# Kernel optimization log

Measured on AMD Instinct MI355X. Metric: run time of the kernel, lower is better.

## Reference

```python
import jax, jax.numpy as jnp
import numpy as np

EMB_DIM = 768
HEADS = 12
HEAD_DIM = EMB_DIM // HEADS  # 64


def setup_inputs() -> dict:
    key = jax.random.key(0)
    ks = jax.random.split(key, 9)
    s = 1.0 / np.sqrt(EMB_DIM)
    d = dict(
        x=jax.random.normal(ks[0], (2, 2048, EMB_DIM), dtype=jnp.float32),
        wq_w=jax.random.normal(ks[1], (EMB_DIM, EMB_DIM), dtype=jnp.float32) * s,
        wq_b=jax.random.normal(ks[2], (EMB_DIM,), dtype=jnp.float32) * 0.01,
        wk_w=jax.random.normal(ks[3], (EMB_DIM, EMB_DIM), dtype=jnp.float32) * s,
        wk_b=jax.random.normal(ks[4], (EMB_DIM,), dtype=jnp.float32) * 0.01,
        wv_w=jax.random.normal(ks[5], (EMB_DIM, EMB_DIM), dtype=jnp.float32) * s,
        wv_b=jax.random.normal(ks[6], (EMB_DIM,), dtype=jnp.float32) * 0.01,
        wo_w=jax.random.normal(ks[7], (EMB_DIM, EMB_DIM), dtype=jnp.float32) * s,
        wo_b=jax.random.normal(ks[8], (EMB_DIM,), dtype=jnp.float32) * 0.01,
    )
    return d


def reference(x, wq_w, wq_b, wk_w, wk_b, wv_w, wv_b, wo_w, wo_b):
    b, n, _ = x.shape
    # Linear projections (torch Linear: x @ W^T + b). q scaled by 1/8 == 1/sqrt(head_dim).
    q = (x @ wq_w.T + wq_b) / 8.0
    k = x @ wk_w.T + wk_b
    v = x @ wv_w.T + wv_b
    # [b, h, n, d]
    q = q.reshape(b, n, HEADS, HEAD_DIM).transpose(0, 2, 1, 3)
    k = k.reshape(b, n, HEADS, HEAD_DIM).transpose(0, 2, 1, 3)
    v = v.reshape(b, n, HEADS, HEAD_DIM).transpose(0, 2, 1, 3)
    # Full [b, h, n, n] score matrix with causal mask (strict upper triangle = -inf)
    scores = jnp.einsum('bhqd,bhkd->bhqk', q, k)
    causal = jnp.tril(jnp.ones((n, n), dtype=bool))  # True where allowed
    scores = jnp.where(causal[None, None], scores, -jnp.inf)
    attn = jax.nn.softmax(scores, axis=-1)
    out = jnp.einsum('bhqk,bhkd->bhqd', attn, v)
    out = out.transpose(0, 2, 1, 3).reshape(b, n, EMB_DIM)
    return out @ wo_w.T + wo_b
```

## Files before the change

### kernel.cpp

```cpp
#include <hip/hip_runtime.h>
#include <hip/hip_bf16.h>
#include <math.h>

#define EMB  768
#define NH   12
#define HD   64
#define SEQ  2048
#define BATCH 2
#define NTOK 4096

typedef __attribute__((ext_vector_type(8))) short short8;
typedef __attribute__((ext_vector_type(4))) float float4v;

static __device__ __forceinline__ short f2bf(float f) {
    __hip_bfloat16 h = __float2bfloat16(f);
    return *reinterpret_cast<short*>(&h);
}

static __device__ __forceinline__ void gll16(const void* g, void* l) {
    __builtin_amdgcn_global_load_lds(
        (const __attribute__((address_space(1))) void*)g,
        (__attribute__((address_space(3))) void*)l, 16, 0, 0);
}

__device__ const unsigned char UB[40] = {
    3,4,5,6,7,8,9,10,11,12,13,14,15,
    7,8,9,10,11,12,13,14,15,
    11,12,13,14,15,
    15,
    2,6,10,14,
    1,5,9,13,
    0,4,8,12};
__device__ const unsigned char UC[40] = {
    0,0,0,0,0,0,0,0,0,0,0,0,0,
    1,1,1,1,1,1,1,1,1,
    2,2,2,2,2,
    3,
    0,1,2,3,
    0,1,2,3,
    0,1,2,3};

__global__ __launch_bounds__(256) void cast_kernel(
    const float* __restrict__ x,  const float* __restrict__ wq,
    const float* __restrict__ wk, const float* __restrict__ wv,
    const float* __restrict__ wo,
    __hip_bfloat16* __restrict__ xb,  __hip_bfloat16* __restrict__ wqb,
    __hip_bfloat16* __restrict__ wkb, __hip_bfloat16* __restrict__ wvb,
    __hip_bfloat16* __restrict__ wob)
{
    const size_t S0 = (size_t)NTOK * EMB;
    const size_t S1 = (size_t)EMB * EMB;
    size_t i = ((size_t)blockIdx.x * 256 + threadIdx.x) * 8;
    const float* src; __hip_bfloat16* dst; size_t off;
    if      (i < S0)            { src = x;  dst = xb;  off = i; }
    else if (i < S0 + S1)       { src = wq; dst = wqb; off = i - S0; }
    else if (i < S0 + 2 * S1)   { src = wk; dst = wkb; off = i - S0 - S1; }
    else if (i < S0 + 3 * S1)   { src = wv; dst = wvb; off = i - S0 - 2 * S1; }
    else                        { src = wo; dst = wob; off = i - S0 - 3 * S1; }
    float4 f0 = *(const float4*)&src[off];
    float4 f1 = *(const float4*)&src[off + 4];
    short8 o;
    o[0] = f2bf(f0.x); o[1] = f2bf(f0.y); o[2] = f2bf(f0.z); o[3] = f2bf(f0.w);
    o[4] = f2bf(f1.x); o[5] = f2bf(f1.y); o[6] = f2bf(f1.z); o[7] = f2bf(f1.w);
    *(short8*)&dst[off] = o;
}

__global__ __launch_bounds__(256) void qkv_mfma_kernel(
    const __hip_bfloat16* __restrict__ xb,
    const __hip_bfloat16* __restrict__ wqb, const float* __restrict__ bq,
    const __hip_bfloat16* __restrict__ wkb, const float* __restrict__ bk,
    const __hip_bfloat16* __restrict__ wvb, const float* __restrict__ bv,
    __hip_bfloat16* __restrict__ q, __hip_bfloat16* __restrict__ k,
    __hip_bfloat16* __restrict__ vT)
{
    __shared__ __align__(16) short SM[12288];
    short* As = SM;
    short* Bs = SM + 4096;
    const int t = threadIdx.x;
    const int w = t >> 6, lane = t & 63;
    const int col = lane & 15, quad = lane >> 4;
    const int wm = w >> 1, wn = w & 1;
    const int m0 = blockIdx.y * 64;
    const int mat = blockIdx.x / 6;
    const int jj0 = (blockIdx.x % 6) * 128;
    const short* X = (const short*)xb;
    const short* W = (const short*)((mat == 0) ? wqb : (mat == 1) ? wkb : wvb);
    const float* bias = (mat == 0) ? bq : (mat == 1) ? bk : bv;

    float4v acc[2][4];
    #pragma unroll
    for (int mi = 0; mi < 2; ++mi)
        #pragma unroll
        for (int ni = 0; ni < 4; ++ni) acc[mi][ni] = (float4v){0.f, 0.f, 0.f, 0.f};

    for (int kb = 0; kb < EMB; kb += 64) {
        #pragma unroll
        for (int c = 0; c < 2; ++c) {
            int I = w * 128 + c * 64 + lane;
            int row = I >> 3;
            int c8 = (I & 7) ^ (row & 7);
            gll16(X + (size_t)(m0 + row) * EMB + kb + c8 * 8,
                  &As[(w * 128 + c * 64) * 8]);
        }
        #pragma unroll
        for (int c = 0; c < 4; ++c) {
            int I = w * 256 + c * 64 + lane;
            int row = I >> 3;
            int c8 = (I & 7) ^ (row & 7);
            gll16(W + (size_t)(jj0 + row) * EMB + kb + c8 * 8,
                  &Bs[(w * 256 + c * 64) * 8]);
        }
        __syncthreads();
        #pragma unroll
        for (int ks = 0; ks < 2; ++ks) {
            short8 a[2], b[4];
            #pragma unroll
            for (int mi = 0; mi < 2; ++mi) {
                int row = wm * 32 + mi * 16 + col;
                a[mi] = *(short8*)&As[row * 64 + (((ks * 4 + quad) ^ (row & 7)) * 8)];
            }
            #pragma unroll
            for (int ni = 0; ni < 4; ++ni) {
                int row = wn * 64 + ni * 16 + col;
                b[ni] = *(short8*)&Bs[row * 64 + (((ks * 4 + quad) ^ (row & 7)) * 8)];
            }
            #pragma unroll
            for (int mi = 0; mi < 2; ++mi)
                #pragma unroll
                for (int ni = 0; ni < 4; ++ni)
                    acc[mi][ni] = __builtin_amdgcn_mfma_f32_16x16x32_bf16(
                        a[mi], b[ni], acc[mi][ni], 0, 0, 0);
        }
        __syncthreads();
    }
    const int bi = m0 >> 11, n0g = m0 & (SEQ - 1);
    if (mat != 2) {
        const float scale = (mat == 0) ? 0.125f * 1.44269504088896f : 1.0f;
        __hip_bfloat16* dstqk = (mat == 0) ? q : k;
        #pragma unroll
        for (int mi = 0; mi < 2; ++mi)
            #pragma unroll
            for (int ni = 0; ni < 4; ++ni) {
                int gj_l = wn * 64 + ni * 16 + col;
                float bsv = bias[jj0 + gj_l];
                #pragma unroll
                for (int r = 0; r < 4; ++r) {
                    int n_l = wm * 32 + mi * 16 + quad * 4 + r;
                    int cswz = (gj_l >> 3) ^ (n_l & 15);
                    SM[(n_l << 7) + (cswz << 3) + (gj_l & 7)] =
                        f2bf((acc[mi][ni][r] + bsv) * scale);
                }
            }
        __syncthreads();
        #pragma unroll
        for (int it = 0; it < 4; ++it) {
            int I = it * 256 + t;
            int n_l = I >> 4, c = I & 15;
            short8 val = *(short8*)&SM[(n_l << 7) + ((c ^ (n_l & 15)) << 3)];
            int gj = jj0 + c * 8;
            int h = gj >> 6, d0 = gj & 63;
            int gm = m0 + n_l;
            int bb = gm >> 11, n = gm & (SEQ - 1);
            *(short8*)&dstqk[(((size_t)bb * NH + h) * SEQ + n) * HD + d0] = val;
        }
    } else {
        #pragma unroll
        for (int mi = 0; mi < 2; ++mi)
            #pragma unroll
            for (int ni = 0; ni < 4; ++ni) {
                int d_l = wn * 64 + ni * 16 + col;
                float bsv = bias[jj0 + d_l];
                #pragma unroll
                for (int r = 0; r < 4; ++r) {
                    int n_l = wm * 32 + mi * 16 + quad * 4 + r;
                    int cn = n_l >> 3;
                    SM[(d_l << 6) + (((cn ^ (d_l & 7))) << 3) + (n_l & 7)] =
                        f2bf(acc[mi][ni][r] + bsv);
                }
            }
        __syncthreads();
        #pragma unroll
        for (int it = 0; it < 4; ++it) {
            int I = it * 256 + t;
            int d_l = I >> 3, cn = I & 7;
            short8 val = *(short8*)&SM[(d_l << 6) + ((cn ^ (d_l & 7)) << 3)];
            int gj = jj0 + d_l;
            int h = gj >> 6, dd = gj & 63;
            *(short8*)&vT[(((size_t)bi * NH + h) * HD + dd) * SEQ + n0g + cn * 8] = val;
        }
    }
}

__global__ __launch_bounds__(256) void attn_mfma_kernel(
    const __hip_bfloat16* __restrict__ qg, const __hip_bfloat16* __restrict__ kg,
    const __hip_bfloat16* __restrict__ vTg, __hip_bfloat16* __restrict__ ao,
    float* __restrict__ Osp, float* __restrict__ lsp)
{
    __shared__ __align__(16) short Ks[2][64 * 64];
    __shared__ __align__(16) short Vt[2][64 * 64];
    __shared__ __align__(16) short Ps[4][32][72];
    const int t = threadIdx.x;
    const int w = t >> 6, lane = t & 63;
    const int col = lane & 15, quad = lane >> 4;
    const int id = blockIdx.x;
    const int bh = id % 24;
    const int x = id / 24;
    const int b = UB[x], c = UC[x];
    const int kt0 = c * 8;
    const int tottiles = 2 * b + 2;
    const int niter = (tottiles - kt0 < 8) ? (tottiles - kt0) : 8;
    const bool single = (b <= 3);
    const int q0 = b * 128;
    const size_t base = (size_t)bh * SEQ * HD;
    const short* kp = (const short*)kg + base;
    const short* vp = (const short*)vTg + base;
    const short* qp = (const short*)qg + base;

    short8 qa[2][2];
    #pragma unroll
    for (int mi = 0; mi < 2; ++mi) {
        int qrow = q0 + (2 * w + mi) * 16 + col;
        #pragma unroll
        for (int ks = 0; ks < 2; ++ks)
            qa[mi][ks] = *(const short8*)&qp[(size_t)qrow * HD + ks * 32 + quad * 8];
    }
    float4v accO[2][4];
    float lacc[2][4];
    #pragma unroll
    for (int mi = 0; mi < 2; ++mi) {
        #pragma unroll
        for (int di = 0; di < 4; ++di) accO[mi][di] = (float4v){0.f, 0.f, 0.f, 0.f};
        #pragma unroll
        for (int r = 0; r < 4; ++r) lacc[mi][r] = 0.f;
    }

    {
        const int k0 = kt0 * 64;
        #pragma unroll
        for (int cc = 0; cc < 2; ++cc) {
            int I = w * 128 + cc * 64 + lane;
            int row = I >> 3;
            int c8 = (I & 7) ^ (row & 7);
            gll16(kp + (size_t)(k0 + row) * HD + c8 * 8, &Ks[0][(w * 128 + cc * 64) * 8]);
            gll16(vp + (size_t)row * SEQ + k0 + c8 * 8, &Vt[0][(w * 128 + cc * 64) * 8]);
        }
    }

    for (int lk = 0; lk < niter; ++lk) {
        const int kt = kt0 + lk;
        const int cur = lk & 1;
        const int k0 = kt * 64;
        __syncthreads();
        if (lk + 1 < niter) {
            const int kn = k0 + 64;
            #pragma unroll
            for (int cc = 0; cc < 2; ++cc) {
                int I = w * 128 + cc * 64 + lane;
                int row = I >> 3;
                int c8 = (I & 7) ^ (row & 7);
                gll16(kp + (size_t)(kn + row) * HD + c8 * 8,
                      &Ks[cur ^ 1][(w * 128 + cc * 64) * 8]);
                gll16(vp + (size_t)row * SEQ + kn + c8 * 8,
                      &Vt[cur ^ 1][(w * 128 + cc * 64) * 8]);
            }
        }
        const short* Kc = &Ks[cur][0];
        const short* Vc = &Vt[cur][0];

        float4v s[2][4];
        #pragma unroll
        for (int mi = 0; mi < 2; ++mi)
            #pragma unroll
            for (int ni = 0; ni < 4; ++ni) s[mi][ni] = (float4v){0.f, 0.f, 0.f, 0.f};
        #pragma unroll
        for (int ks = 0; ks < 2; ++ks)
            #pragma unroll
            for (int ni = 0; ni < 4; ++ni) {
                int row = ni * 16 + col;
                short8 kf = *(short8*)&Kc[row * 64 + (((ks * 4 + quad) ^ (row & 7)) * 8)];
                #pragma unroll
                for (int mi = 0; mi < 2; ++mi)
                    s[mi][ni] = __builtin_amdgcn_mfma_f32_16x16x32_bf16(
                        qa[mi][ks], kf, s[mi][ni], 0, 0, 0);
            }

        if (k0 >= q0) {
            #pragma unroll
            for (int mi = 0; mi < 2; ++mi)
                #pragma unroll
                for (int ni = 0; ni < 4; ++ni) {
                    int gcol = k0 + ni * 16 + col;
                    #pragma unroll
                    for (int r = 0; r < 4; ++r) {
                        int grow = q0 + (2 * w + mi) * 16 + quad * 4 + r;
                        s[mi][ni][r] = (gcol > grow) ? 0.f : exp2f(s[mi][ni][r]);
                    }
                }
        } else {
            #pragma unroll
            for (int mi = 0; mi < 2; ++mi)
                #pragma unroll
                for (int ni = 0; ni < 4; ++ni)
                    #pragma unroll
                    for (int r = 0; r < 4; ++r)
                        s[mi][ni][r] = exp2f(s[mi][ni][r]);
        }
        #pragma unroll
        for (int mi = 0; mi < 2; ++mi)
            #pragma unroll
            for (int r = 0; r < 4; ++r)
                lacc[mi][r] += (s[mi][0][r] + s[mi][1][r]) + (s[mi][2][r] + s[mi][3][r]);

        #pragma unroll
        for (int mi = 0; mi < 2; ++mi)
            #pragma unroll
            for (int ni = 0; ni < 4; ++ni)
                #pragma unroll
                for (int r = 0; r < 4; ++r)
                    Ps[w][mi * 16 + quad * 4 + r][ni * 16 + col] = f2bf(s[mi][ni][r]);
        short8 pa[2][2];
        #pragma unroll
        for (int mi = 0; mi < 2; ++mi)
            #pragma unroll
            for (int ks = 0; ks < 2; ++ks)
                pa[mi][ks] = *(short8*)&Ps[w][mi * 16 + col][ks * 32 + quad * 8];

        #pragma unroll
        for (int ks = 0; ks < 2; ++ks)
            #pragma unroll
            for (int di = 0; di < 4; ++di) {
                int row = di * 16 + col;
                short8 vf = *(short8*)&Vc[row * 64 + (((ks * 4 + quad) ^ (row & 7)) * 8)];
                #pragma unroll
                for (int mi = 0; mi < 2; ++mi)
                    accO[mi][di] = __builtin_amdgcn_mfma_f32_16x16x32_bf16(
                        pa[mi][ks], vf, accO[mi][di], 0, 0, 0);
            }
    }

    #pragma unroll
    for (int msk = 1; msk < 16; msk <<= 1)
        #pragma unroll
        for (int mi = 0; mi < 2; ++mi)
            #pragma unroll
            for (int r = 0; r < 4; ++r)
                lacc[mi][r] += __shfl_xor(lacc[mi][r], msk);

    const int bi = bh / NH, h = bh % NH;
    if (single) {
        #pragma unroll
        for (int mi = 0; mi < 2; ++mi)
            #pragma unroll
            for (int r = 0; r < 4; ++r) {
                float inv = 1.0f / lacc[mi][r];
                int n = q0 + (2 * w + mi) * 16 + quad * 4 + r;
                #pragma unroll
                for (int di = 0; di < 4; ++di)
                    ao[((size_t)bi * SEQ + n) * EMB + h * HD + di * 16 + col] =
                        __float2bfloat16(accO[mi][di][r] * inv);
            }
    } else {
        float* Os = Osp + (size_t)c * 2 * 1536 * EMB;
        float* ls = lsp + (size_t)c * 2 * 1536 * NH;
        #pragma unroll
        for (int mi = 0; mi < 2; ++mi)
            #pragma unroll
            for (int r = 0; r < 4; ++r) {
                int n = q0 + (2 * w + mi) * 16 + quad * 4 + r;
                int nn = n - 512;
                size_t rowb = ((size_t)bi * 1536 + nn) * EMB + h * HD;
                #pragma unroll
                for (int di = 0; di < 4; ++di)
                    Os[rowb + di * 16 + col] = accO[mi][di][r];
                if (col == 0)
                    ls[((size_t)bi * 1536 + nn) * NH + h] = lacc[mi][r];
            }
    }
}

__global__ __launch_bounds__(256) void combine_kernel(
    const float* __restrict__ Osp, const float* __restrict__ lsp,
    __hip_bfloat16* __restrict__ ao)
{
    const size_t SLOT = (size_t)2 * 1536 * EMB;
    const size_t LSLOT = (size_t)2 * 1536 * NH;
    size_t e8 = ((size_t)blockIdx.x * 256 + threadIdx.x) * 8;
    int u = e8 / EMB;
    int within = e8 % EMB;
    int h = within >> 6;
    int bi = u / 1536, nn = u % 1536;
    int n = 512 + nn;
    int qb = n >> 7;
    int nc = (2 * qb + 9) >> 3;
    float4 a0 = *(const float4*)&Osp[e8];
    float4 a1 = *(const float4*)&Osp[e8 + 4];
    float lsum = lsp[(size_t)u * NH + h];
    for (int cc = 1; cc < nc; ++cc) {
        const float* O = Osp + (size_t)cc * SLOT;
        float4 b0 = *(const float4*)&O[e8];
        float4 b1 = *(const float4*)&O[e8 + 4];
        a0.x += b0.x; a0.y += b0.y; a0.z += b0.z; a0.w += b0.w;
        a1.x += b1.x; a1.y += b1.y; a1.z += b1.z; a1.w += b1.w;
        lsum += lsp[(size_t)cc * LSLOT + (size_t)u * NH + h];
    }
    float inv = 1.0f / lsum;
    short8 o;
    o[0] = f2bf(a0.x * inv); o[1] = f2bf(a0.y * inv);
    o[2] = f2bf(a0.z * inv); o[3] = f2bf(a0.w * inv);
    o[4] = f2bf(a1.x * inv); o[5] = f2bf(a1.y * inv);
    o[6] = f2bf(a1.z * inv); o[7] = f2bf(a1.w * inv);
    *(short8*)&ao[((size_t)bi * SEQ + n) * EMB + within] = o;
}

__global__ __launch_bounds__(256) void out_proj_mfma_kernel(
    const __hip_bfloat16* __restrict__ a, const __hip_bfloat16* __restrict__ wob,
    const float* __restrict__ bias, float* __restrict__ out)
{
    __shared__ __align__(16) short As[64 * 64];
    __shared__ __align__(16) short Bs[64 * 64];
    const int t = threadIdx.x;
    const int w = t >> 6, lane = t & 63;
    const int col = lane & 15, quad = lane >> 4;
    const int wm = w >> 1, wn = w & 1;
    const int m0 = blockIdx.y * 64;
    const int n0 = blockIdx.x * 64;
    const short* A = (const short*)a;
    const short* W = (const short*)wob;

    float4v acc[2][2];
    #pragma unroll
    for (int mi = 0; mi < 2; ++mi)
        #pragma unroll
        for (int ni = 0; ni < 2; ++ni) acc[mi][ni] = (float4v){0.f, 0.f, 0.f, 0.f};

    for (int kb = 0; kb < EMB; kb += 64) {
        #pragma unroll
        for (int c = 0; c < 2; ++c) {
            int I = w * 128 + c * 64 + lane;
            int row = I >> 3;
            int c8 = (I & 7) ^ (row & 7);
            gll16(A + (size_t)(m0 + row) * EMB + kb + c8 * 8,
                  &As[(w * 128 + c * 64) * 8]);
            gll16(W + (size_t)(n0 + row) * EMB + kb + c8 * 8,
                  &Bs[(w * 128 + c * 64) * 8]);
        }
        __syncthreads();
        #pragma unroll
        for (int ks = 0; ks < 2; ++ks) {
            short8 av[2], bv[2];
            #pragma unroll
            for (int mi = 0; mi < 2; ++mi) {
                int row = wm * 32 + mi * 16 + col;
                av[mi] = *(short8*)&As[row * 64 + (((ks * 4 + quad) ^ (row & 7)) * 8)];
            }
            #pragma unroll
            for (int ni = 0; ni < 2; ++ni) {
                int row = wn * 32 + ni * 16 + col;
                bv[ni] = *(short8*)&Bs[row * 64 + (((ks * 4 + quad) ^ (row & 7)) * 8)];
            }
            #pragma unroll
            for (int mi = 0; mi < 2; ++mi)
                #pragma unroll
                for (int ni = 0; ni < 2; ++ni)
                    acc[mi][ni] = __builtin_amdgcn_mfma_f32_16x16x32_bf16(
                        av[mi], bv[ni], acc[mi][ni], 0, 0, 0);
        }
        __syncthreads();
    }
    #pragma unroll
    for (int mi = 0; mi < 2; ++mi)
        #pragma unroll
        for (int ni = 0; ni < 2; ++ni) {
            int gj = n0 + wn * 32 + ni * 16 + col;
            float bsv = bias[gj];
            #pragma unroll
            for (int r = 0; r < 4; ++r) {
                int gm = m0 + wm * 32 + mi * 16 + quad * 4 + r;
                out[(size_t)gm * EMB + gj] = acc[mi][ni][r] + bsv;
            }
        }
}

extern "C" void kernel_launch(void* const* d_in, const int* in_sizes, int n_in,
                              void* d_out, int out_size, void* d_ws, size_t ws_size,
                              hipStream_t stream) {
    const float* x  = (const float*)d_in[0];
    const float* wq = (const float*)d_in[1];
    const float* bq = (const float*)d_in[2];
    const float* wk = (const float*)d_in[3];
    const float* bk = (const float*)d_in[4];
    const float* wv = (const float*)d_in[5];
    const float* bv = (const float*)d_in[6];
    const float* wo = (const float*)d_in[7];
    const float* bo = (const float*)d_in[8];
    float* out = (float*)d_out;

    const size_t TOK = (size_t)NTOK * EMB;
    const size_t WSZ = (size_t)EMB * EMB;
    __hip_bfloat16* xb  = (__hip_bfloat16*)d_ws;
    __hip_bfloat16* wqb = xb  + TOK;
    __hip_bfloat16* wkb = wqb + WSZ;
    __hip_bfloat16* wvb = wkb + WSZ;
    __hip_bfloat16* wob = wvb + WSZ;
    __hip_bfloat16* qb  = wob + WSZ;
    __hip_bfloat16* kb  = qb  + TOK;
    __hip_bfloat16* vTb = kb  + TOK;
    __hip_bfloat16* aob = vTb + TOK;
    float* Osp = (float*)(aob + TOK);
    float* lsp = Osp + (size_t)4 * 2 * 1536 * EMB;

    cast_kernel<<<2688, 256, 0, stream>>>(x, wq, wk, wv, wo, xb, wqb, wkb, wvb, wob);
    qkv_mfma_kernel<<<dim3(18, 64), 256, 0, stream>>>(xb, wqb, bq, wkb, bk, wvb, bv,
                                                      qb, kb, vTb);
    attn_mfma_kernel<<<960, 256, 0, stream>>>(qb, kb, vTb, aob, Osp, lsp);
    combine_kernel<<<1152, 256, 0, stream>>>(Osp, lsp, aob);
    out_proj_mfma_kernel<<<dim3(12, 64), 256, 0, stream>>>(aob, wob, bo, out);
}
```

Baseline: 160.6 us.

## Fuse split-KV combine into output projection A-tile loading

Removes the separate combine kernel. For rows that have split partial results, the output projection kernel now sums the fp32 partial O slots and l sums itself, normalizes, converts to bf16 and writes the A tile into LDS. This saves one launch and the bf16 round trip through global memory. In exchange, every column block re-reads and re-reduces the fp32 partials, so partial-buffer traffic grows about twelvefold, and these A loads become synchronous register loads instead of direct-to-LDS loads.

Measured after the change: 192.3 us. +19.7%, slower.

```diff
diff --git a/kernel.cpp b/kernel.cpp
--- a/kernel.cpp
+++ b/kernel.cpp
@@ -378,54 +378,43 @@
     }
 }
 
-__global__ __launch_bounds__(256) void combine_kernel(
-    const float* __restrict__ Osp, const float* __restrict__ lsp,
-    __hip_bfloat16* __restrict__ ao)
-{
-    const size_t SLOT = (size_t)2 * 1536 * EMB;
-    const size_t LSLOT = (size_t)2 * 1536 * NH;
-    size_t e8 = ((size_t)blockIdx.x * 256 + threadIdx.x) * 8;
-    int u = e8 / EMB;
-    int within = e8 % EMB;
-    int h = within >> 6;
-    int bi = u / 1536, nn = u % 1536;
-    int n = 512 + nn;
-    int qb = n >> 7;
-    int nc = (2 * qb + 9) >> 3;
-    float4 a0 = *(const float4*)&Osp[e8];
-    float4 a1 = *(const float4*)&Osp[e8 + 4];
-    float lsum = lsp[(size_t)u * NH + h];
-    for (int cc = 1; cc < nc; ++cc) {
-        const float* O = Osp + (size_t)cc * SLOT;
-        float4 b0 = *(const float4*)&O[e8];
-        float4 b1 = *(const float4*)&O[e8 + 4];
-        a0.x += b0.x; a0.y += b0.y; a0.z += b0.z; a0.w += b0.w;
-        a1.x += b1.x; a1.y += b1.y; a1.z += b1.z; a1.w += b1.w;
-        lsum += lsp[(size_t)cc * LSLOT + (size_t)u * NH + h];
-    }
-    float inv = 1.0f / lsum;
-    short8 o;
-    o[0] = f2bf(a0.x * inv); o[1] = f2bf(a0.y * inv);
-    o[2] = f2bf(a0.z * inv); o[3] = f2bf(a0.w * inv);
-    o[4] = f2bf(a1.x * inv); o[5] = f2bf(a1.y * inv);
-    o[6] = f2bf(a1.z * inv); o[7] = f2bf(a1.w * inv);
-    *(short8*)&ao[((size_t)bi * SEQ + n) * EMB + within] = o;
-}
-
 __global__ __launch_bounds__(256) void out_proj_mfma_kernel(
-    const __hip_bfloat16* __restrict__ a, const __hip_bfloat16* __restrict__ wob,
+    const __hip_bfloat16* __restrict__ a, const float* __restrict__ Osp,
+    const float* __restrict__ lsp, const __hip_bfloat16* __restrict__ wob,
     const float* __restrict__ bias, float* __restrict__ out)
 {
     __shared__ __align__(16) short As[64 * 64];
     __shared__ __align__(16) short Bs[64 * 64];
+    __shared__ float invL[12 * 64];
+    const size_t SLOT  = (size_t)2 * 1536 * EMB;
+    const size_t LSLOT = (size_t)2 * 1536 * NH;
     const int t = threadIdx.x;
     const int w = t >> 6, lane = t & 63;
     const int col = lane & 15, quad = lane >> 4;
     const int wm = w >> 1, wn = w & 1;
     const int m0 = blockIdx.y * 64;
     const int n0 = blockIdx.x * 64;
+    const int bi = m0 >> 11;
+    const int nrow0 = m0 & (SEQ - 1);
+    const bool part = (nrow0 >= 512);
     const short* A = (const short*)a;
     const short* W = (const short*)wob;
+
+    int nc = 0; size_t ubase = 0;
+    if (part) {
+        int qb = nrow0 >> 7;
+        nc = (2 * qb + 9) >> 3;
+        ubase = (size_t)bi * 1536 + (nrow0 - 512);
+        for (int i = t; i < 12 * 64; i += 256) {
+            int h = i >> 6, row = i & 63;
+            size_t u = ubase + row;
+            float ls = lsp[u * NH + h];
+            for (int cc = 1; cc < nc; ++cc)
+                ls += lsp[(size_t)cc * LSLOT + u * NH + h];
+            invL[i] = 1.0f / ls;
+        }
+        __syncthreads();
+    }
 
     float4v acc[2][2];
     #pragma unroll
@@ -434,13 +423,46 @@
         for (int ni = 0; ni < 2; ++ni) acc[mi][ni] = (float4v){0.f, 0.f, 0.f, 0.f};
 
     for (int kb = 0; kb < EMB; kb += 64) {
+        const int h = kb >> 6;
+        if (!part) {
+            #pragma unroll
+            for (int c = 0; c < 2; ++c) {
+                int I = w * 128 + c * 64 + lane;
+                int row = I >> 3;
+                int c8 = (I & 7) ^ (row & 7);
+                gll16(A + (size_t)(m0 + row) * EMB + kb + c8 * 8,
+                      &As[(w * 128 + c * 64) * 8]);
+            }
+        } else {
+            #pragma unroll
+            for (int c = 0; c < 2; ++c) {
+                int I = w * 128 + c * 64 + lane;
+                int row = I >> 3;
+                int c8 = (I & 7) ^ (row & 7);
+                size_t off = (ubase + row) * EMB + kb + c8 * 8;
+                float4 s0 = *(const float4*)&Osp[off];
+                float4 s1 = *(const float4*)&Osp[off + 4];
+                for (int cc = 1; cc < nc; ++cc) {
+                    const float* O = Osp + (size_t)cc * SLOT;
+                    float4 b0 = *(const float4*)&O[off];
+                    float4 b1 = *(const float4*)&O[off + 4];
+                    s0.x += b0.x; s0.y += b0.y; s0.z += b0.z; s0.w += b0.w;
+                    s1.x += b1.x; s1.y += b1.y; s1.z += b1.z; s1.w += b1.w;
+                }
+                float inv = invL[h * 64 + row];
+                short8 v8;
+                v8[0] = f2bf(s0.x * inv); v8[1] = f2bf(s0.y * inv);
+                v8[2] = f2bf(s0.z * inv); v8[3] = f2bf(s0.w * inv);
+                v8[4] = f2bf(s1.x * inv); v8[5] = f2bf(s1.y * inv);
+                v8[6] = f2bf(s1.z * inv); v8[7] = f2bf(s1.w * inv);
+                *(short8*)&As[(size_t)I * 8] = v8;
+            }
+        }
         #pragma unroll
         for (int c = 0; c < 2; ++c) {
             int I = w * 128 + c * 64 + lane;
             int row = I >> 3;
             int c8 = (I & 7) ^ (row & 7);
-            gll16(A + (size_t)(m0 + row) * EMB + kb + c8 * 8,
-                  &As[(w * 128 + c * 64) * 8]);
             gll16(W + (size_t)(n0 + row) * EMB + kb + c8 * 8,
                   &Bs[(w * 128 + c * 64) * 8]);
         }
@@ -513,6 +535,5 @@
     qkv_mfma_kernel<<<dim3(18, 64), 256, 0, stream>>>(xb, wqb, bq, wkb, bk, wvb, bv,
                                                       qb, kb, vTb);
     attn_mfma_kernel<<<960, 256, 0, stream>>>(qb, kb, vTb, aob, Osp, lsp);
-    combine_kernel<<<1152, 256, 0, stream>>>(Osp, lsp, aob);
-    out_proj_mfma_kernel<<<dim3(12, 64), 256, 0, stream>>>(aob, wob, bo, out);
-}
+    out_proj_mfma_kernel<<<dim3(12, 64), 256, 0, stream>>>(aob, Osp, lsp, wob, bo, out);
+}
```
